# Performance work log

Hardware: AMD Instinct MI355X
Metric: run time of the kernel (lower is better)

Reference implementation:

```python
import jax, jax.numpy as jnp
import numpy as np

DIM = 512
MOVE_EMBED_DIM = 64
NUM_BUCKETS = 64
EMBED = 768
B = 8192
STEPS = 10


def setup_inputs() -> dict:
    key = jax.random.key(0)
    ks = jax.random.split(key, 16)
    def g(i, shape, scale=0.02):
        return jax.random.normal(ks[i], shape, jnp.float32) * scale
    return {
        "boards": jax.random.normal(ks[0], (STEPS, B, EMBED), jnp.float32),
        "flags": jax.random.randint(ks[1], (STEPS - 2, B), 0, 2).astype(bool),
        "themes": jax.random.randint(ks[2], (B,), 0, 10),
        "moves": jax.random.randint(ks[3], (B,), 0, NUM_BUCKETS),
        "start": jax.random.uniform(ks[4], (DIM,), jnp.float32),
        "red_w": g(5, (DIM, EMBED)), "red_b": jnp.zeros((DIM,), jnp.float32),
        "ca_w": g(6, (DIM, DIM)), "ca_b": jnp.zeros((DIM,), jnp.float32),
        "cb_w": g(7, (DIM, DIM)), "cb_b": jnp.zeros((DIM,), jnp.float32),
        "move_emb": g(8, (NUM_BUCKETS, MOVE_EMBED_DIM), 1.0),
        "fc1_w": g(9, (DIM, DIM + MOVE_EMBED_DIM)), "fc1_b": jnp.zeros((DIM,), jnp.float32),
        "fc2_w": g(10, (DIM, DIM)), "fc2_b": jnp.zeros((DIM,), jnp.float32),
        "fc3_w": g(11, (1024, DIM)), "fc3_b": jnp.zeros((1024,), jnp.float32),
        "fc4_w": g(12, (1024, 1024)), "fc4_b": jnp.zeros((1024,), jnp.float32),
        "fc5_w": g(13, (512, 1024)), "fc5_b": jnp.zeros((512,), jnp.float32),
        "out_w": g(14, (1, 512)), "out_b": jnp.zeros((1,), jnp.float32),
    }


def reference(boards, flags, themes, moves, start, red_w, red_b, ca_w, ca_b,
              cb_w, cb_b, move_emb, fc1_w, fc1_b, fc2_w, fc2_b, fc3_w, fc3_b,
              fc4_w, fc4_b, fc5_w, fc5_b, out_w, out_b):
    bsz = boards.shape[1]
    # boards[0:2] are never masked; boards[2:10] are zeroed where flags are False
    full_flags = jnp.concatenate([jnp.ones((2, bsz), bool), flags], axis=0)  # [10,B]
    emb = jnp.where(full_flags[:, :, None], boards, 0.0)                     # [10,B,E]
    # shared dim reducer + relu applied to all 10 positions at once
    e = jax.nn.relu(jnp.einsum('sbe,de->sbd', emb, red_w) + red_b)           # [10,B,DIM]
    # precompute combiner_b contribution for every step (batched GEMM)
    eb = jnp.einsum('sbd,kd->sbk', e, cb_w) + cb_b                           # [10,B,DIM]
    # combiner_a(start)+combiner_b(e0) == combiner_a(h0)+... with h0 = start broadcast
    h0 = jnp.broadcast_to(start, (bsz, DIM))
    def step(h, eb_t):
        return jnp.tanh(h @ ca_w.T + ca_b + eb_t), None
    h, _ = jax.lax.scan(step, h0, eb)                                        # [B,DIM]
    # dropout layers are identity in eval mode
    m = move_emb[moves]                                                      # [B,MOVE_EMBED_DIM]
    x = jax.nn.relu(jnp.concatenate([h, m], axis=-1) @ fc1_w.T + fc1_b)
    x = jax.nn.relu(x @ fc2_w.T + fc2_b)
    x = jax.nn.relu(x @ fc3_w.T + fc3_b)
    x = jax.nn.relu(x @ fc4_w.T + fc4_b)
    x = jax.nn.relu(x @ fc5_w.T + fc5_b)
    return x @ out_w.T + out_b                                               # [B,1]
```

## Files before the change

### kernel.cpp

```cpp
#include <hip/hip_runtime.h>
#include <math.h>

#define BATCH  8192
#define EMBED  768
#define DIMD   512
#define MEDIM  64
#define NSTEP  10

typedef __bf16 bf16x8 __attribute__((ext_vector_type(8)));
typedef float  f32x4  __attribute__((ext_vector_type(4)));

__device__ __forceinline__ void load16_lds(const void* g, void* l)
{
    auto* gp = (__attribute__((address_space(1))) char*)(uintptr_t)g;
    auto* lp = (__attribute__((address_space(3))) char*)(unsigned int)(uintptr_t)l;
    __builtin_amdgcn_global_load_lds(gp, lp, 16, 0, 0);
}

#define BN 128
#define BK 32

template<int ACT, bool ADDEB, bool GATHER, int BMT>
__global__ __launch_bounds__(256)
void gemm_bf16(const __bf16* __restrict__ A, const __bf16* __restrict__ Bt,
               const float* __restrict__ bias, const __bf16* __restrict__ add,
               const __bf16* __restrict__ me, const int* __restrict__ moves,
               __bf16* __restrict__ C, int M, int N, int K)
{
    constexpr int NG = (BMT + BN) / 16;
    constexpr int AG = BMT / 16;
    constexpr int MR = BMT / 32;

    __shared__ __bf16 lds[2][(BMT + BN) * BK];

    const int nwg  = gridDim.x * gridDim.y;
    const int orig = blockIdx.y * gridDim.x + blockIdx.x;
    const int cpx  = nwg >> 3;
    const int swz  = (orig & 7) * cpx + (orig >> 3);
    const int bx   = swz % gridDim.x;
    const int by   = swz / gridDim.x;

    const int tid  = threadIdx.x;
    const int wave = tid >> 6;
    const int lane = tid & 63;
    const int row0 = by * BMT;
    const int col0 = bx * BN;

    const int wr = (wave >> 1) * (BMT / 2);
    const int wc = (wave & 1) * 64;
    const int fr = lane & 15;
    const int q  = lane >> 4;

    const int srow = lane >> 2;
    const int skk  = (((lane & 3) ^ ((lane >> 3) & 3)) * 8);

    auto stage = [&](int buf, int k0) {
#pragma unroll
        for (int ci = 0; ci < NG / 4; ++ci) {
            const int c = ci * 4 + wave;
            const int r = c * 16 + srow;
            const __bf16* g;
            if (c < AG) {
                if (GATHER) {
                    const int grow = row0 + r;
                    g = (k0 < DIMD)
                        ? (A  + (size_t)grow * DIMD + k0 + skk)
                        : (me + (size_t)moves[grow] * MEDIM + (k0 - DIMD) + skk);
                } else {
                    g = A + (size_t)(row0 + r) * K + k0 + skk;
                }
            } else {
                g = Bt + (size_t)(col0 + (r - BMT)) * K + k0 + skk;
            }
            load16_lds(g, &lds[buf][c * 512]);
        }
    };

    auto frag = [&](const __bf16* base, int r) -> bf16x8 {
        return *(const bf16x8*)&base[r * 32 + ((q ^ ((r >> 1) & 3)) << 3)];
    };

    f32x4 acc[MR][4] = {};

    stage(0, 0);
    __syncthreads();

    const int NT = K / BK;
    int cur = 0;
    for (int t = 0; t < NT; ++t) {
        if (t + 1 < NT) stage(cur ^ 1, (t + 1) * BK);

        const __bf16* As = lds[cur];
        const __bf16* Bs = lds[cur] + BMT * BK;
        bf16x8 af[MR], bfr[4];
#pragma unroll
        for (int m = 0; m < MR; ++m)
            af[m] = frag(As, wr + m * 16 + fr);
#pragma unroll
        for (int n = 0; n < 4; ++n)
            bfr[n] = frag(Bs, wc + n * 16 + fr);
#pragma unroll
        for (int m = 0; m < MR; ++m)
#pragma unroll
            for (int n = 0; n < 4; ++n)
                acc[m][n] = __builtin_amdgcn_mfma_f32_16x16x32_bf16(
                                af[m], bfr[n], acc[m][n], 0, 0, 0);
        __syncthreads();
        cur ^= 1;
    }

#pragma unroll
    for (int m = 0; m < MR; ++m) {
#pragma unroll
        for (int n = 0; n < 4; ++n) {
            const int cc = col0 + wc + n * 16 + fr;
            const float bb = bias[cc];
#pragma unroll
            for (int j = 0; j < 4; ++j) {
                const int rr = row0 + wr + m * 16 + (lane >> 4) * 4 + j;
                float v = acc[m][n][j] + bb;
                if (ADDEB) v += (float)add[(size_t)rr * N + cc];
                if (ACT == 1) v = fmaxf(v, 0.0f);
                if (ACT == 2) {
                    const float p = __expf(2.0f * v);
                    v = 1.0f - 2.0f / (p + 1.0f);
                }
                C[(size_t)rr * N + cc] = (__bf16)v;
            }
        }
    }
}

__global__ __launch_bounds__(256)
void cvt_boards_all(const float* __restrict__ src, const int* __restrict__ flags,
                    __bf16* __restrict__ dst)
{
    const int idx  = blockIdx.x * 256 + threadIdx.x;
    const int grow = idx / 96;
    const int s    = grow >> 13;
    const int b    = grow & 8191;
    float m = 1.0f;
    if (s >= 2) m = flags[(size_t)(s - 2) * BATCH + b] ? 1.0f : 0.0f;
    const float4 v0 = ((const float4*)src)[(size_t)idx * 2];
    const float4 v1 = ((const float4*)src)[(size_t)idx * 2 + 1];
    bf16x8 o;
    o[0] = (__bf16)(v0.x * m); o[1] = (__bf16)(v0.y * m);
    o[2] = (__bf16)(v0.z * m); o[3] = (__bf16)(v0.w * m);
    o[4] = (__bf16)(v1.x * m); o[5] = (__bf16)(v1.y * m);
    o[6] = (__bf16)(v1.z * m); o[7] = (__bf16)(v1.w * m);
    *(bf16x8*)(dst + (size_t)idx * 8) = o;
}

enum : int { W_RED = 0, W_CA = 393216, W_CB = 655360, W_FC1 = 917504,
             W_FC2 = 1212416, W_FC3 = 1474560, W_FC4 = 1998848,
             W_FC5 = 3047424, W_ME = 3571712, W_TOTAL = 3575808 };

__global__ __launch_bounds__(256)
void cvt_weights(const float* __restrict__ w0, const float* __restrict__ w1,
                 const float* __restrict__ w2, const float* __restrict__ w3,
                 const float* __restrict__ w4, const float* __restrict__ w5,
                 const float* __restrict__ w6, const float* __restrict__ w7,
                 const float* __restrict__ w8, __bf16* __restrict__ dst)
{
    const int idx = blockIdx.x * 256 + threadIdx.x;
    if (idx >= W_TOTAL / 8) return;
    const int e = idx * 8;
    const float* src; int off;
    if      (e < W_CA)  { src = w0; off = W_RED; }
    else if (e < W_CB)  { src = w1; off = W_CA; }
    else if (e < W_FC1) { src = w2; off = W_CB; }
    else if (e < W_FC2) { src = w3; off = W_FC1; }
    else if (e < W_FC3) { src = w4; off = W_FC2; }
    else if (e < W_FC4) { src = w5; off = W_FC3; }
    else if (e < W_FC5) { src = w6; off = W_FC4; }
    else if (e < W_ME)  { src = w7; off = W_FC5; }
    else                { src = w8; off = W_ME; }
    const float4 v0 = ((const float4*)(src + (e - off)))[0];
    const float4 v1 = ((const float4*)(src + (e - off)))[1];
    bf16x8 o;
    o[0] = (__bf16)v0.x; o[1] = (__bf16)v0.y; o[2] = (__bf16)v0.z; o[3] = (__bf16)v0.w;
    o[4] = (__bf16)v1.x; o[5] = (__bf16)v1.y; o[6] = (__bf16)v1.z; o[7] = (__bf16)v1.w;
    *(bf16x8*)(dst + (size_t)e) = o;
}

__global__ __launch_bounds__(256)
void gemv_start(const float* __restrict__ caw, const float* __restrict__ cab,
                const float* __restrict__ start, float* __restrict__ tmp)
{
    __shared__ float s[DIMD];
    for (int i = threadIdx.x; i < DIMD; i += 256) s[i] = start[i];
    __syncthreads();
    const int n = blockIdx.x * 256 + threadIdx.x;
    const float4* w = (const float4*)(caw + (size_t)n * DIMD);
    float acc = 0.0f;
#pragma unroll 8
    for (int k = 0; k < DIMD / 4; ++k) {
        const float4 wv = w[k];
        acc += wv.x * s[k * 4] + wv.y * s[k * 4 + 1] +
               wv.z * s[k * 4 + 2] + wv.w * s[k * 4 + 3];
    }
    tmp[n] = acc + cab[n];
}

__global__ __launch_bounds__(256)
void h1_init(const float* __restrict__ tmp, const __bf16* __restrict__ eb0,
             __bf16* __restrict__ h)
{
    const int idx = blockIdx.x * 256 + threadIdx.x;
    const int c8 = idx & 63;
    const bf16x8 e = ((const bf16x8*)eb0)[idx];
    bf16x8 o;
#pragma unroll
    for (int j = 0; j < 8; ++j) {
        const float v = tmp[c8 * 8 + j] + (float)e[j];
        const float p = __expf(2.0f * v);
        o[j] = (__bf16)(1.0f - 2.0f / (p + 1.0f));
    }
    ((bf16x8*)h)[idx] = o;
}

__global__ __launch_bounds__(256)
void out_head(const __bf16* __restrict__ x, const float* __restrict__ out_w,
              const float* __restrict__ out_b, float* __restrict__ out)
{
    const int wid  = threadIdx.x >> 6;
    const int lane = threadIdx.x & 63;
    const int row  = blockIdx.x * 4 + wid;
    const bf16x8 xv = *(const bf16x8*)(x + (size_t)row * DIMD + lane * 8);
    const float4 w0 = ((const float4*)out_w)[lane * 2];
    const float4 w1 = ((const float4*)out_w)[lane * 2 + 1];
    float s = (float)xv[0] * w0.x + (float)xv[1] * w0.y + (float)xv[2] * w0.z +
              (float)xv[3] * w0.w + (float)xv[4] * w1.x + (float)xv[5] * w1.y +
              (float)xv[6] * w1.z + (float)xv[7] * w1.w;
#pragma unroll
    for (int off = 32; off; off >>= 1) s += __shfl_down(s, off, 64);
    if (lane == 0) out[row] = s + out_b[0];
}

extern "C" void kernel_launch(void* const* d_in, const int* in_sizes, int n_in,
                              void* d_out, int out_size, void* d_ws, size_t ws_size,
                              hipStream_t stream)
{
    const float* boards  = (const float*)d_in[0];
    const int*   flags   = (const int*)  d_in[1];
    const int*   moves   = (const int*)  d_in[3];
    const float* start   = (const float*)d_in[4];
    const float* red_w   = (const float*)d_in[5];
    const float* red_b   = (const float*)d_in[6];
    const float* ca_w    = (const float*)d_in[7];
    const float* ca_b    = (const float*)d_in[8];
    const float* cb_w    = (const float*)d_in[9];
    const float* cb_b    = (const float*)d_in[10];
    const float* move_emb= (const float*)d_in[11];
    const float* fc1_w   = (const float*)d_in[12];
    const float* fc1_b   = (const float*)d_in[13];
    const float* fc2_w   = (const float*)d_in[14];
    const float* fc2_b   = (const float*)d_in[15];
    const float* fc3_w   = (const float*)d_in[16];
    const float* fc3_b   = (const float*)d_in[17];
    const float* fc4_w   = (const float*)d_in[18];
    const float* fc4_b   = (const float*)d_in[19];
    const float* fc5_w   = (const float*)d_in[20];
    const float* fc5_b   = (const float*)d_in[21];
    const float* out_w   = (const float*)d_in[22];
    const float* out_b   = (const float*)d_in[23];

    __bf16* wsb = (__bf16*)d_ws;
    __bf16* wpool  = wsb;
    __bf16* b_all  = wsb + 3575808;
    __bf16* e_all  = wsb + 66490368;
    __bf16* eb_all = wsb + 108433408;
    __bf16* hA     = wsb + 150376448;
    __bf16* hB     = wsb + 154570752;
    float*  tmpv   = (float*)(wsb + 158765056);
    __bf16* x1     = wsb + 159789056;
    __bf16* x2     = wsb + 163983360;
    __bf16* x3     = wsb + 168177664;
    __bf16* x4     = wsb + 176566272;
    __bf16* x5     = wsb + 184954880;

    const dim3 blk(256);

    cvt_weights<<<1746, blk, 0, stream>>>(red_w, ca_w, cb_w, fc1_w, fc2_w,
                                          fc3_w, fc4_w, fc5_w, move_emb, wpool);
    cvt_boards_all<<<30720, blk, 0, stream>>>(boards, flags, b_all);
    gemv_start<<<2, blk, 0, stream>>>(ca_w, ca_b, start, tmpv);

    gemm_bf16<1, false, false, 128><<<dim3(4, 640), blk, 0, stream>>>(
        b_all, wpool + W_RED, red_b, nullptr, nullptr, nullptr, e_all,
        NSTEP * BATCH, DIMD, EMBED);
    gemm_bf16<0, false, false, 128><<<dim3(4, 640), blk, 0, stream>>>(
        e_all, wpool + W_CB, cb_b, nullptr, nullptr, nullptr, eb_all,
        NSTEP * BATCH, DIMD, DIMD);

    h1_init<<<2048, blk, 0, stream>>>(tmpv, eb_all, hA);

    __bf16* hcur = hA;
    __bf16* hnxt = hB;
    for (int s = 1; s < NSTEP; ++s) {
        const __bf16* ebs = eb_all + (size_t)s * BATCH * DIMD;
        gemm_bf16<2, true, false, 64><<<dim3(4, 128), blk, 0, stream>>>(
            hcur, wpool + W_CA, ca_b, ebs, nullptr, nullptr, hnxt,
            BATCH, DIMD, DIMD);
        __bf16* t = hcur; hcur = hnxt; hnxt = t;
    }

    gemm_bf16<1, false, true, 128><<<dim3(4, 64), blk, 0, stream>>>(
        hcur, wpool + W_FC1, fc1_b, nullptr, wpool + W_ME, moves, x1,
        BATCH, DIMD, DIMD + MEDIM);
    gemm_bf16<1, false, false, 128><<<dim3(4, 64), blk, 0, stream>>>(
        x1, wpool + W_FC2, fc2_b, nullptr, nullptr, nullptr, x2, BATCH, DIMD, DIMD);
    gemm_bf16<1, false, false, 128><<<dim3(8, 64), blk, 0, stream>>>(
        x2, wpool + W_FC3, fc3_b, nullptr, nullptr, nullptr, x3, BATCH, 1024, DIMD);
    gemm_bf16<1, false, false, 128><<<dim3(8, 64), blk, 0, stream>>>(
        x3, wpool + W_FC4, fc4_b, nullptr, nullptr, nullptr, x4, BATCH, 1024, 1024);
    gemm_bf16<1, false, false, 128><<<dim3(4, 64), blk, 0, stream>>>(
        x4, wpool + W_FC5, fc5_b, nullptr, nullptr, nullptr, x5, BATCH, DIMD, 1024);

    out_head<<<BATCH / 4, blk, 0, stream>>>(x5, out_w, out_b, (float*)d_out);
}
```

Baseline: 470.5 us.

## Triple-buffer GEMM LDS staging with explicit vmcnt waits and hoisted gather indices

Replaces the double-buffered global-to-LDS pipeline with a three-stage ring, issuing loads two K-tiles ahead. Partial s_waitcnt vmcnt waits let later tiles stay in flight, replacing full __syncthreads drains. It also hoists the moves[] index loads for the gathered fc1 operand out of the staging loop into registers. The cost is 50% more LDS per block, which may lower occupancy, and correctness now depends on hand-counted vmcnt values.

```diff
diff --git a/kernel.cpp b/kernel.cpp
--- a/kernel.cpp
+++ b/kernel.cpp
@@ -17,6 +17,8 @@
     __builtin_amdgcn_global_load_lds(gp, lp, 16, 0, 0);
 }
 
+#define WAITV(n) asm volatile("s_waitcnt vmcnt(" #n ")" ::: "memory")
+
 #define BN 128
 #define BK 32
 
@@ -30,8 +32,9 @@
     constexpr int NG = (BMT + BN) / 16;
     constexpr int AG = BMT / 16;
     constexpr int MR = BMT / 32;
-
-    __shared__ __bf16 lds[2][(BMT + BN) * BK];
+    constexpr int NC = NG / 4;
+
+    __shared__ __bf16 lds[3][(BMT + BN) * BK];
 
     const int nwg  = gridDim.x * gridDim.y;
     const int orig = blockIdx.y * gridDim.x + blockIdx.x;
@@ -54,18 +57,24 @@
     const int srow = lane >> 2;
     const int skk  = (((lane & 3) ^ ((lane >> 3) & 3)) * 8);
 
+    int mv[2] = {0, 0};
+    if (GATHER) {
+#pragma unroll
+        for (int ci = 0; ci < 2; ++ci)
+            mv[ci] = moves[row0 + (ci * 4 + wave) * 16 + srow];
+    }
+
     auto stage = [&](int buf, int k0) {
 #pragma unroll
-        for (int ci = 0; ci < NG / 4; ++ci) {
+        for (int ci = 0; ci < NC; ++ci) {
             const int c = ci * 4 + wave;
             const int r = c * 16 + srow;
             const __bf16* g;
             if (c < AG) {
                 if (GATHER) {
-                    const int grow = row0 + r;
                     g = (k0 < DIMD)
-                        ? (A  + (size_t)grow * DIMD + k0 + skk)
-                        : (me + (size_t)moves[grow] * MEDIM + (k0 - DIMD) + skk);
+                        ? (A  + (size_t)(row0 + r) * DIMD + k0 + skk)
+                        : (me + (size_t)mv[ci] * MEDIM + (k0 - DIMD) + skk);
                 } else {
                     g = A + (size_t)(row0 + r) * K + k0 + skk;
                 }
@@ -82,16 +91,31 @@
 
     f32x4 acc[MR][4] = {};
 
+    const int NT = K / BK;
     stage(0, 0);
-    __syncthreads();
-
-    const int NT = K / BK;
-    int cur = 0;
+    stage(1, BK);
+
+    int rd = 0;
     for (int t = 0; t < NT; ++t) {
-        if (t + 1 < NT) stage(cur ^ 1, (t + 1) * BK);
-
-        const __bf16* As = lds[cur];
-        const __bf16* Bs = lds[cur] + BMT * BK;
+        if (t + 2 < NT) {
+            int wrb = rd + 2; if (wrb >= 3) wrb -= 3;
+            stage(wrb, (t + 2) * BK);
+        }
+        const int infl = (NT - 1 - t >= 2) ? 2 : (NT - 1 - t);
+        if constexpr (NC == 4) {
+            if (infl == 2)      WAITV(8);
+            else if (infl == 1) WAITV(4);
+            else                WAITV(0);
+        } else {
+            if (infl == 2)      WAITV(6);
+            else if (infl == 1) WAITV(3);
+            else                WAITV(0);
+        }
+        __builtin_amdgcn_s_barrier();
+        __builtin_amdgcn_sched_barrier(0);
+
+        const __bf16* As = lds[rd];
+        const __bf16* Bs = lds[rd] + BMT * BK;
         bf16x8 af[MR], bfr[4];
 #pragma unroll
         for (int m = 0; m < MR; ++m)
@@ -105,8 +129,10 @@
             for (int n = 0; n < 4; ++n)
                 acc[m][n] = __builtin_amdgcn_mfma_f32_16x16x32_bf16(
                                 af[m], bfr[n], acc[m][n], 0, 0, 0);
-        __syncthreads();
-        cur ^= 1;
+
+        __builtin_amdgcn_s_barrier();
+        __builtin_amdgcn_sched_barrier(0);
+        ++rd; if (rd >= 3) rd -= 3;
     }
 
 #pragma unroll
```

Measured after the change: 443.1 us. -5.8%, faster.
